# Optimization experiments

Hardware: AMD Instinct MI355X
Metric: run time of the kernel (lower is better)

Reference implementation:

```python
import jax, jax.numpy as jnp
import numpy as np

VOCAB = 50000
E = 32            # embed_size; node state is E x E
LABELS = 10
DEPTH = 11        # perfect binary tree: 2^DEPTH - 1 = 2047 nodes, 1024 leaves
N_NODES = 2 ** DEPTH - 1
LN_EPS = 1e-5


def setup_inputs() -> dict:
    key = jax.random.key(0)
    ks = jax.random.split(key, 8)
    word_ids = jax.random.randint(ks[0], (N_NODES,), 0, VOCAB, dtype=jnp.int32)
    label = 3
    emb_table = jax.random.normal(ks[1], (VOCAB, E * E), dtype=jnp.float32) * 0.02
    Ww = jax.random.normal(ks[2], (E, E), dtype=jnp.float32) * (1.0 / np.sqrt(E))
    Wb = jax.random.normal(ks[3], (E,), dtype=jnp.float32) * 0.01
    gamma = jnp.ones((E, E), dtype=jnp.float32)   # LayerNorm((1,E,E)) affine weight
    beta = jnp.zeros((E, E), dtype=jnp.float32)
    Pw = jax.random.normal(ks[4], (LABELS, E * E), dtype=jnp.float32) * (1.0 / E)
    Pb = jnp.zeros((LABELS,), dtype=jnp.float32)
    return {"word_ids": word_ids, "label": label, "emb_table": emb_table,
            "Ww": Ww, "Wb": Wb, "gamma": gamma, "beta": beta, "Pw": Pw, "Pb": Pb}


def reference(word_ids, label, emb_table, Ww, Wb, gamma, beta, Pw, Pb):
    # word_ids: level-order ids of a perfect binary tree, children of within-level
    # index j at level d are indices 2j, 2j+1 at level d+1.
    embs = emb_table[word_ids].reshape(N_NODES, E, E)  # [N, E, E]

    def ln_relu(x):
        # torch LayerNorm((1,E,E)): normalize over the whole E*E matrix, affine per element
        mu = jnp.mean(x, axis=(1, 2), keepdims=True)
        var = jnp.var(x, axis=(1, 2), keepdims=True)
        y = (x - mu) * jax.lax.rsqrt(var + LN_EPS) * gamma + beta
        return jax.nn.relu(y)

    # leaves: level DEPTH-1
    start = 2 ** (DEPTH - 1) - 1
    h = ln_relu(embs[start:])  # [2^(DEPTH-1), E, E]
    # internal levels bottom-up; loop over fixed DEPTH-1 levels (not data dims)
    for d in range(DEPTH - 2, -1, -1):
        s = 2 ** d - 1
        cur = embs[s:s + 2 ** d]                     # [n_d, E, E]
        l, r = h[0::2], h[1::2]                      # children pairs
        x = jnp.einsum('nij,njk,nkl->nil', l, r, cur)
        x = x @ Ww.T + Wb                            # Linear applied row-wise
        h = ln_relu(x)

    root = h[0].reshape(-1)                          # [E*E]
    logits = root @ Pw.T + Pb                        # [LABELS]
    prediction = jnp.argmax(logits)
    loss = -jax.nn.log_softmax(logits)[label]
    return (prediction, loss)
```

## Files before the change

kernel.cpp:

```cpp
#include <hip/hip_runtime.h>
#include <hip/hip_bf16.h>

#define LN_EPS 1e-5f
#define TSB 40
#define TILEB (32 * TSB)
#define MAGIC 0x5A5A7E1Du

typedef __attribute__((ext_vector_type(8))) short bf16x8;
typedef __attribute__((ext_vector_type(16))) float f32x16;

__device__ __forceinline__ short bf16b(float f) {
  return __builtin_bit_cast(short, __float2bfloat16(f));
}

__device__ __forceinline__ void wave_reduce2(float& s1, float& s2) {
  #pragma unroll
  for (int off = 32; off; off >>= 1) {
    s1 += __shfl_xor(s1, off);
    s2 += __shfl_xor(s2, off);
  }
}

__device__ __forceinline__ bf16x8 frag_ld(const short* t, int l, int k0) {
  return *(const bf16x8*)&t[(l & 31) * TSB + ((l >> 5) << 3) + k0];
}

__device__ __forceinline__ int cd_row(int r, int l) {
  return (r & 3) + 8 * (r >> 2) + 4 * (l >> 5);
}

__device__ __forceinline__ void cd_store(short* t, int l, const f32x16 d,
                                         bool transp) {
  const int col = l & 31;
  if (transp) {
    #pragma unroll
    for (int r = 0; r < 16; ++r) t[col * TSB + cd_row(r, l)] = bf16b(d[r]);
  } else {
    #pragma unroll
    for (int r = 0; r < 16; ++r) t[cd_row(r, l) * TSB + col] = bf16b(d[r]);
  }
}

struct NodeParams {
  bf16x8 w0, w1;
  float wb;
  float ga[16], be[16];
};

__device__ __forceinline__ NodeParams load_params(const float* __restrict__ Ww,
    const float* __restrict__ Wb, const float* __restrict__ gamma,
    const float* __restrict__ beta, int l) {
  NodeParams P;
  const int n = l & 31, kh = (l >> 5) * 8;
  float w[8];
  *(float4*)&w[0] = *(const float4*)&Ww[n * 32 + kh];
  *(float4*)&w[4] = *(const float4*)&Ww[n * 32 + kh + 4];
  #pragma unroll
  for (int i = 0; i < 8; ++i) P.w0[i] = bf16b(w[i]);
  *(float4*)&w[0] = *(const float4*)&Ww[n * 32 + kh + 16];
  *(float4*)&w[4] = *(const float4*)&Ww[n * 32 + kh + 20];
  #pragma unroll
  for (int i = 0; i < 8; ++i) P.w1[i] = bf16b(w[i]);
  P.wb = Wb[n];
  #pragma unroll
  for (int r = 0; r < 16; ++r) {
    const int idx = cd_row(r, l) * 32 + n;
    P.ga[r] = gamma[idx];
    P.be[r] = beta[idx];
  }
  return P;
}

__device__ __forceinline__ f32x16 mm32(const short* A, const short* B, int l) {
  f32x16 acc = {};
  acc = __builtin_amdgcn_mfma_f32_32x32x16_bf16(frag_ld(A, l, 0),
                                                frag_ld(B, l, 0), acc, 0, 0, 0);
  acc = __builtin_amdgcn_mfma_f32_32x32x16_bf16(frag_ld(A, l, 16),
                                                frag_ld(B, l, 16), acc, 0, 0, 0);
  return acc;
}

__device__ __forceinline__ void node_mfma(short* A, short* Bt, const short* Ct,
                                          const NodeParams& P, int l,
                                          short* dst, bool transpOut,
                                          float* fout) {
  f32x16 t1 = mm32(A, Bt, l);
  cd_store(A, l, t1, false);
  f32x16 t2 = mm32(A, Ct, l);
  cd_store(Bt, l, t2, false);
  f32x16 x = {};
  x = __builtin_amdgcn_mfma_f32_32x32x16_bf16(frag_ld(Bt, l, 0), P.w0, x, 0, 0, 0);
  x = __builtin_amdgcn_mfma_f32_32x32x16_bf16(frag_ld(Bt, l, 16), P.w1, x, 0, 0, 0);
  float s1 = 0.f, s2 = 0.f;
  #pragma unroll
  for (int r = 0; r < 16; ++r) {
    x[r] += P.wb;
    s1 += x[r];
    s2 += x[r] * x[r];
  }
  wave_reduce2(s1, s2);
  const float mu = s1 * (1.f / 1024.f);
  const float rs = rsqrtf(s2 * (1.f / 1024.f) - mu * mu + LN_EPS);
  #pragma unroll
  for (int r = 0; r < 16; ++r)
    x[r] = fmaxf((x[r] - mu) * rs * P.ga[r] + P.be[r], 0.f);
  if (fout) {
    #pragma unroll
    for (int r = 0; r < 16; ++r) fout[cd_row(r, l) * 32 + (l & 31)] = x[r];
  } else {
    cd_store(dst, l, x, transpOut);
  }
}

__device__ __forceinline__ void stage_f32(short* dst,
                                          const float* __restrict__ src, int l,
                                          bool transp) {
  float v[16];
  #pragma unroll
  for (int q = 0; q < 4; ++q)
    *(float4*)&v[q * 4] = *(const float4*)&src[l * 16 + q * 4];
  const int row = l >> 1, c0 = (l & 1) * 16;
  if (transp) {
    #pragma unroll
    for (int i = 0; i < 16; ++i) dst[(c0 + i) * TSB + row] = bf16b(v[i]);
  } else {
    #pragma unroll
    for (int i = 0; i < 8; ++i) {
      unsigned lo = (unsigned short)bf16b(v[2 * i]);
      unsigned hi = (unsigned short)bf16b(v[2 * i + 1]);
      ((unsigned*)dst)[row * (TSB / 2) + (c0 >> 1) + i] = lo | (hi << 16);
    }
  }
}

__device__ __forceinline__ void lds_put16(short* dst, const short v[16], int l,
                                          bool transp) {
  const int row = l >> 1, c0 = (l & 1) * 16;
  if (transp) {
    #pragma unroll
    for (int i = 0; i < 16; ++i) dst[(c0 + i) * TSB + row] = v[i];
  } else {
    #pragma unroll
    for (int i = 0; i < 8; ++i) {
      unsigned lo = (unsigned short)v[2 * i];
      unsigned hi = (unsigned short)v[2 * i + 1];
      ((unsigned*)dst)[row * (TSB / 2) + (c0 >> 1) + i] = lo | (hi << 16);
    }
  }
}

__device__ __forceinline__ void fetch_tile(short* dstLds,
                                           const unsigned* __restrict__ src,
                                           int l, bool transp) {
  short v[16];
  #pragma unroll
  for (int i = 0; i < 8; ++i) {
    unsigned x = __hip_atomic_load(src + l * 8 + i, __ATOMIC_RELAXED,
                                   __HIP_MEMORY_SCOPE_AGENT);
    v[2 * i] = (short)(x & 0xFFFFu);
    v[2 * i + 1] = (short)(x >> 16);
  }
  lds_put16(dstLds, v, l, transp);
}

__device__ __forceinline__ void emit_tile(unsigned* __restrict__ dst,
                                          const short* t, int u) {
  #pragma unroll
  for (int q = 0; q < 2; ++q) {
    const int w = 2 * u + q;
    const int row = w >> 4, cp = w & 15;
    unsigned v = *(const unsigned*)&t[row * TSB + cp * 2];
    __hip_atomic_store(dst + w, v, __ATOMIC_RELAXED, __HIP_MEMORY_SCOPE_AGENT);
  }
}

__device__ __forceinline__ void flag_set(unsigned* f) {
  __hip_atomic_store(f, MAGIC, __ATOMIC_RELAXED, __HIP_MEMORY_SCOPE_AGENT);
}

__device__ __forceinline__ void flag_wait(const unsigned* f) {
  while (__hip_atomic_load(f, __ATOMIC_RELAXED, __HIP_MEMORY_SCOPE_AGENT) !=
         MAGIC)
    __builtin_amdgcn_s_sleep(1);
  asm volatile("" ::: "memory");
}

__device__ __forceinline__ void leaf_ln(short* dst, const float* __restrict__ src,
                                        const float* __restrict__ gamma,
                                        const float* __restrict__ beta, int l,
                                        bool transp) {
  float v[16], ga[16], be[16];
  #pragma unroll
  for (int q = 0; q < 4; ++q) {
    *(float4*)&v[q * 4] = *(const float4*)&src[l * 16 + q * 4];
    *(float4*)&ga[q * 4] = *(const float4*)&gamma[l * 16 + q * 4];
    *(float4*)&be[q * 4] = *(const float4*)&beta[l * 16 + q * 4];
  }
  float s1 = 0.f, s2 = 0.f;
  #pragma unroll
  for (int i = 0; i < 16; ++i) { s1 += v[i]; s2 += v[i] * v[i]; }
  wave_reduce2(s1, s2);
  const float mu = s1 * (1.f / 1024.f);
  const float rs = rsqrtf(s2 * (1.f / 1024.f) - mu * mu + LN_EPS);
  short o[16];
  #pragma unroll
  for (int i = 0; i < 16; ++i)
    o[i] = bf16b(fmaxf((v[i] - mu) * rs * ga[i] + be[i], 0.f));
  lds_put16(dst, o, l, transp);
}

__device__ __forceinline__ void phase3(
    int blk, int u, int wv, int l, short* pool, const NodeParams& P,
    const int* __restrict__ wid, const float* __restrict__ emb,
    const unsigned* __restrict__ hinu, const unsigned* __restrict__ finf,
    unsigned* __restrict__ houtu, unsigned* __restrict__ foutf,
    int b0, int b1, int b2) {
  stage_f32(pool + (8 + wv) * TILEB,
            emb + (size_t)wid[b0 + 4 * blk + wv] * 1024, l, true);
  if (wv < 2)
    stage_f32(pool + (12 + wv) * TILEB,
              emb + (size_t)wid[b1 + 2 * blk + wv] * 1024, l, true);
  else if (wv == 2)
    stage_f32(pool + 14 * TILEB, emb + (size_t)wid[b2 + blk] * 1024, l, true);
  if (u < 8) flag_wait(finf + 8 * blk + u);
  __syncthreads();
  fetch_tile(pool + 2 * wv * TILEB, hinu + (size_t)(8 * blk + 2 * wv) * 512, l,
             false);
  fetch_tile(pool + (2 * wv + 1) * TILEB,
             hinu + (size_t)(8 * blk + 2 * wv + 1) * 512, l, true);
  __syncthreads();
  node_mfma(pool + 2 * wv * TILEB, pool + (2 * wv + 1) * TILEB,
            pool + (8 + wv) * TILEB, P, l, pool + (8 + wv) * TILEB,
            (wv & 1) != 0, nullptr);
  __syncthreads();
  if (wv < 2)
    node_mfma(pool + (8 + 2 * wv) * TILEB, pool + (9 + 2 * wv) * TILEB,
              pool + (12 + wv) * TILEB, P, l, pool + (12 + wv) * TILEB,
              (wv & 1) != 0, nullptr);
  __syncthreads();
  if (wv == 0)
    node_mfma(pool + 12 * TILEB, pool + 13 * TILEB, pool + 14 * TILEB, P, l,
              pool + 14 * TILEB, false, nullptr);
  __syncthreads();
  emit_tile(houtu + (size_t)blk * 512, pool + 14 * TILEB, u);
  asm volatile("s_waitcnt vmcnt(0)" ::: "memory");
  __syncthreads();
  if (u == 0) flag_set(foutf + blk);
}

__global__ __launch_bounds__(256) void k_tree(
    const int* __restrict__ wid, const float* __restrict__ emb,
    const float* __restrict__ Ww, const float* __restrict__ Wb,
    const float* __restrict__ gamma, const float* __restrict__ beta,
    const float* __restrict__ Pw, const float* __restrict__ Pb,
    const int* __restrict__ label,
    unsigned* __restrict__ h8u, unsigned* __restrict__ h5u,
    unsigned* __restrict__ h2u, unsigned* __restrict__ h8f,
    unsigned* __restrict__ h5f, unsigned* __restrict__ h2f,
    float* __restrict__ out) {
  __shared__ __align__(16) short pool[15 * TILEB];
  __shared__ float rootf[1024];
  __shared__ float lred[10];
  const int u = threadIdx.x, blk = blockIdx.x;
  const int wv = u >> 6, l = u & 63;
  NodeParams P = load_params(Ww, Wb, gamma, beta, l);

  {
    if (wv == 0)
      stage_f32(pool + 4 * TILEB, emb + (size_t)wid[511 + 2 * blk] * 1024, l, true);
    else if (wv == 1)
      stage_f32(pool + 5 * TILEB, emb + (size_t)wid[512 + 2 * blk] * 1024, l, true);
    else if (wv == 2)
      stage_f32(pool + 6 * TILEB, emb + (size_t)wid[255 + blk] * 1024, l, true);
    leaf_ln(pool + wv * TILEB, emb + (size_t)wid[1023 + 4 * blk + wv] * 1024,
            gamma, beta, l, (wv & 1) != 0);
    __syncthreads();
    if (wv < 2)
      node_mfma(pool + 2 * wv * TILEB, pool + (2 * wv + 1) * TILEB,
                pool + (4 + wv) * TILEB, P, l, pool + (4 + wv) * TILEB,
                wv == 1, nullptr);
    __syncthreads();
    if (wv == 0)
      node_mfma(pool + 4 * TILEB, pool + 5 * TILEB, pool + 6 * TILEB, P, l,
                pool + 6 * TILEB, false, nullptr);
    __syncthreads();
    emit_tile(h8u + (size_t)blk * 512, pool + 6 * TILEB, u);
    asm volatile("s_waitcnt vmcnt(0)" ::: "memory");
    __syncthreads();
    if (u == 0) flag_set(h8f + blk);
  }

  if (blk >= 32) return;
  phase3(blk, u, wv, l, pool, P, wid, emb, h8u, h8f, h5u, h5f, 127, 63, 31);

  if (blk >= 4) return;
  phase3(blk, u, wv, l, pool, P, wid, emb, h5u, h5f, h2u, h2f, 15, 7, 3);

  if (blk >= 1) return;
  {
    if (wv == 0) stage_f32(pool + 4 * TILEB, emb + (size_t)wid[1] * 1024, l, true);
    else if (wv == 1) stage_f32(pool + 5 * TILEB, emb + (size_t)wid[2] * 1024, l, true);
    else if (wv == 2) stage_f32(pool + 6 * TILEB, emb + (size_t)wid[0] * 1024, l, true);
    if (u < 4) flag_wait(h2f + u);
    __syncthreads();
    fetch_tile(pool + wv * TILEB, h2u + (size_t)wv * 512, l, (wv & 1) != 0);
    __syncthreads();
    if (wv < 2)
      node_mfma(pool + 2 * wv * TILEB, pool + (2 * wv + 1) * TILEB,
                pool + (4 + wv) * TILEB, P, l, pool + (4 + wv) * TILEB, wv == 1,
                nullptr);
    __syncthreads();
    if (wv == 0)
      node_mfma(pool + 4 * TILEB, pool + 5 * TILEB, pool + 6 * TILEB, P, l,
                nullptr, false, rootf);
    __syncthreads();
    #pragma unroll
    for (int q = 0; q < 3; ++q) {
      const int c = wv + 4 * q;
      if (c < 10) {
        float p = 0.f;
        #pragma unroll
        for (int t = 0; t < 4; ++t) {
          float4 r4 = *(const float4*)&rootf[l * 16 + t * 4];
          float4 w4 = *(const float4*)&Pw[c * 1024 + l * 16 + t * 4];
          p += r4.x * w4.x + r4.y * w4.y + r4.z * w4.z + r4.w * w4.w;
        }
        #pragma unroll
        for (int off = 32; off; off >>= 1) p += __shfl_xor(p, off);
        if (l == 0) lred[c] = p + Pb[c];
      }
    }
    __syncthreads();
    if (u == 0) {
      float mmax = lred[0];
      int am = 0;
      #pragma unroll
      for (int c = 1; c < 10; ++c)
        if (lred[c] > mmax) { mmax = lred[c]; am = c; }
      float sum = 0.f;
      #pragma unroll
      for (int c = 0; c < 10; ++c) sum += expf(lred[c] - mmax);
      const float loss = -(lred[label[0]] - mmax - logf(sum));
      out[0] = (float)am;
      out[1] = loss;
    }
  }
}

extern "C" void kernel_launch(void* const* d_in, const int* in_sizes, int n_in,
                              void* d_out, int out_size, void* d_ws, size_t ws_size,
                              hipStream_t stream) {
  const int* wid = (const int*)d_in[0];
  const int* label = (const int*)d_in[1];
  const float* emb = (const float*)d_in[2];
  const float* Ww = (const float*)d_in[3];
  const float* Wb = (const float*)d_in[4];
  const float* g = (const float*)d_in[5];
  const float* b = (const float*)d_in[6];
  const float* Pw = (const float*)d_in[7];
  const float* Pb = (const float*)d_in[8];
  float* out = (float*)d_out;

  unsigned* h8u = (unsigned*)d_ws;
  unsigned* h5u = h8u + 256 * 512;
  unsigned* h2u = h5u + 32 * 512;
  unsigned* h8f = h2u + 4 * 512;
  unsigned* h5f = h8f + 256;
  unsigned* h2f = h5f + 32;

  k_tree<<<256, 256, 0, stream>>>(wid, emb, Ww, Wb, g, b, Pw, Pb, label,
                                  h8u, h5u, h2u, h8f, h5f, h2f, out);
}
```

Before: 31.73 us.

## Precompute cur·Wᵀ per node and collapse tree into two-phase 32-block kernel

```diff
diff --git a/kernel.cpp b/kernel.cpp
--- a/kernel.cpp
+++ b/kernel.cpp
@@ -80,38 +80,6 @@
   return acc;
 }
 
-__device__ __forceinline__ void node_mfma(short* A, short* Bt, const short* Ct,
-                                          const NodeParams& P, int l,
-                                          short* dst, bool transpOut,
-                                          float* fout) {
-  f32x16 t1 = mm32(A, Bt, l);
-  cd_store(A, l, t1, false);
-  f32x16 t2 = mm32(A, Ct, l);
-  cd_store(Bt, l, t2, false);
-  f32x16 x = {};
-  x = __builtin_amdgcn_mfma_f32_32x32x16_bf16(frag_ld(Bt, l, 0), P.w0, x, 0, 0, 0);
-  x = __builtin_amdgcn_mfma_f32_32x32x16_bf16(frag_ld(Bt, l, 16), P.w1, x, 0, 0, 0);
-  float s1 = 0.f, s2 = 0.f;
-  #pragma unroll
-  for (int r = 0; r < 16; ++r) {
-    x[r] += P.wb;
-    s1 += x[r];
-    s2 += x[r] * x[r];
-  }
-  wave_reduce2(s1, s2);
-  const float mu = s1 * (1.f / 1024.f);
-  const float rs = rsqrtf(s2 * (1.f / 1024.f) - mu * mu + LN_EPS);
-  #pragma unroll
-  for (int r = 0; r < 16; ++r)
-    x[r] = fmaxf((x[r] - mu) * rs * P.ga[r] + P.be[r], 0.f);
-  if (fout) {
-    #pragma unroll
-    for (int r = 0; r < 16; ++r) fout[cd_row(r, l) * 32 + (l & 31)] = x[r];
-  } else {
-    cd_store(dst, l, x, transpOut);
-  }
-}
-
 __device__ __forceinline__ void stage_f32(short* dst,
                                           const float* __restrict__ src, int l,
                                           bool transp) {
@@ -133,6 +101,43 @@
   }
 }
 
+__device__ __forceinline__ void cw_prep(short* slot,
+                                        const float* __restrict__ src,
+                                        const NodeParams& P, int l) {
+  stage_f32(slot, src, l, false);
+  f32x16 cw = {};
+  cw = __builtin_amdgcn_mfma_f32_32x32x16_bf16(frag_ld(slot, l, 0), P.w0, cw, 0, 0, 0);
+  cw = __builtin_amdgcn_mfma_f32_32x32x16_bf16(frag_ld(slot, l, 16), P.w1, cw, 0, 0, 0);
+  cd_store(slot, l, cw, true);
+}
+
+__device__ __forceinline__ void node2(short* A, short* Bt, short* CWt,
+                                      const NodeParams& P, int l, short* dst,
+                                      bool transpOut, float* fout) {
+  f32x16 t1 = mm32(A, Bt, l);
+  cd_store(A, l, t1, false);
+  f32x16 x = mm32(A, CWt, l);
+  float s1 = 0.f, s2 = 0.f;
+  #pragma unroll
+  for (int r = 0; r < 16; ++r) {
+    x[r] += P.wb;
+    s1 += x[r];
+    s2 += x[r] * x[r];
+  }
+  wave_reduce2(s1, s2);
+  const float mu = s1 * (1.f / 1024.f);
+  const float rs = rsqrtf(s2 * (1.f / 1024.f) - mu * mu + LN_EPS);
+  #pragma unroll
+  for (int r = 0; r < 16; ++r)
+    x[r] = fmaxf((x[r] - mu) * rs * P.ga[r] + P.be[r], 0.f);
+  if (fout) {
+    #pragma unroll
+    for (int r = 0; r < 16; ++r) fout[cd_row(r, l) * 32 + (l & 31)] = x[r];
+  } else {
+    cd_store(dst, l, x, transpOut);
+  }
+}
+
 __device__ __forceinline__ void lds_put16(short* dst, const short v[16], int l,
                                           bool transp) {
   const int row = l >> 1, c0 = (l & 1) * 16;
@@ -163,15 +168,11 @@
   lds_put16(dstLds, v, l, transp);
 }
 
-__device__ __forceinline__ void emit_tile(unsigned* __restrict__ dst,
-                                          const short* t, int u) {
-  #pragma unroll
-  for (int q = 0; q < 2; ++q) {
-    const int w = 2 * u + q;
-    const int row = w >> 4, cp = w & 15;
-    unsigned v = *(const unsigned*)&t[row * TSB + cp * 2];
-    __hip_atomic_store(dst + w, v, __ATOMIC_RELAXED, __HIP_MEMORY_SCOPE_AGENT);
-  }
+__device__ __forceinline__ void emit512(unsigned* __restrict__ dst,
+                                        const short* t, int u) {
+  const int row = u >> 4, cp = u & 15;
+  unsigned v = *(const unsigned*)&t[row * TSB + cp * 2];
+  __hip_atomic_store(dst + u, v, __ATOMIC_RELAXED, __HIP_MEMORY_SCOPE_AGENT);
 }
 
 __device__ __forceinline__ void flag_set(unsigned* f) {
@@ -209,141 +210,143 @@
   lds_put16(dst, o, l, transp);
 }
 
-__device__ __forceinline__ void phase3(
-    int blk, int u, int wv, int l, short* pool, const NodeParams& P,
-    const int* __restrict__ wid, const float* __restrict__ emb,
-    const unsigned* __restrict__ hinu, const unsigned* __restrict__ finf,
-    unsigned* __restrict__ houtu, unsigned* __restrict__ foutf,
-    int b0, int b1, int b2) {
-  stage_f32(pool + (8 + wv) * TILEB,
-            emb + (size_t)wid[b0 + 4 * blk + wv] * 1024, l, true);
-  if (wv < 2)
-    stage_f32(pool + (12 + wv) * TILEB,
-              emb + (size_t)wid[b1 + 2 * blk + wv] * 1024, l, true);
-  else if (wv == 2)
-    stage_f32(pool + 14 * TILEB, emb + (size_t)wid[b2 + blk] * 1024, l, true);
-  if (u < 8) flag_wait(finf + 8 * blk + u);
-  __syncthreads();
-  fetch_tile(pool + 2 * wv * TILEB, hinu + (size_t)(8 * blk + 2 * wv) * 512, l,
-             false);
-  fetch_tile(pool + (2 * wv + 1) * TILEB,
-             hinu + (size_t)(8 * blk + 2 * wv + 1) * 512, l, true);
-  __syncthreads();
-  node_mfma(pool + 2 * wv * TILEB, pool + (2 * wv + 1) * TILEB,
-            pool + (8 + wv) * TILEB, P, l, pool + (8 + wv) * TILEB,
-            (wv & 1) != 0, nullptr);
-  __syncthreads();
-  if (wv < 2)
-    node_mfma(pool + (8 + 2 * wv) * TILEB, pool + (9 + 2 * wv) * TILEB,
-              pool + (12 + wv) * TILEB, P, l, pool + (12 + wv) * TILEB,
-              (wv & 1) != 0, nullptr);
-  __syncthreads();
-  if (wv == 0)
-    node_mfma(pool + 12 * TILEB, pool + 13 * TILEB, pool + 14 * TILEB, P, l,
-              pool + 14 * TILEB, false, nullptr);
-  __syncthreads();
-  emit_tile(houtu + (size_t)blk * 512, pool + 14 * TILEB, u);
-  asm volatile("s_waitcnt vmcnt(0)" ::: "memory");
-  __syncthreads();
-  if (u == 0) flag_set(foutf + blk);
-}
-
-__global__ __launch_bounds__(256) void k_tree(
+__global__ __launch_bounds__(512) void k_tree2(
     const int* __restrict__ wid, const float* __restrict__ emb,
     const float* __restrict__ Ww, const float* __restrict__ Wb,
     const float* __restrict__ gamma, const float* __restrict__ beta,
     const float* __restrict__ Pw, const float* __restrict__ Pb,
-    const int* __restrict__ label,
-    unsigned* __restrict__ h8u, unsigned* __restrict__ h5u,
-    unsigned* __restrict__ h2u, unsigned* __restrict__ h8f,
-    unsigned* __restrict__ h5f, unsigned* __restrict__ h2f,
-    float* __restrict__ out) {
-  __shared__ __align__(16) short pool[15 * TILEB];
-  __shared__ float rootf[1024];
-  __shared__ float lred[10];
+    const int* __restrict__ label, unsigned* __restrict__ h5u,
+    unsigned* __restrict__ h5f, float* __restrict__ out) {
+  extern __shared__ __align__(16) short pool[];
   const int u = threadIdx.x, blk = blockIdx.x;
   const int wv = u >> 6, l = u & 63;
   NodeParams P = load_params(Ww, Wb, gamma, beta, l);
 
+  cw_prep(pool + (2 * wv) * TILEB,
+          emb + (size_t)wid[511 + 16 * blk + 2 * wv] * 1024, P, l);
+  cw_prep(pool + (2 * wv + 1) * TILEB,
+          emb + (size_t)wid[512 + 16 * blk + 2 * wv] * 1024, P, l);
+  cw_prep(pool + (16 + wv) * TILEB,
+          emb + (size_t)wid[255 + 8 * blk + wv] * 1024, P, l);
+  if (wv < 4)
+    cw_prep(pool + (24 + wv) * TILEB,
+            emb + (size_t)wid[127 + 4 * blk + wv] * 1024, P, l);
+  else if (wv < 6)
+    cw_prep(pool + (28 + (wv - 4)) * TILEB,
+            emb + (size_t)wid[63 + 2 * blk + (wv - 4)] * 1024, P, l);
+  else if (wv == 6)
+    cw_prep(pool + 30 * TILEB, emb + (size_t)wid[31 + blk] * 1024, P, l);
+
   {
-    if (wv == 0)
-      stage_f32(pool + 4 * TILEB, emb + (size_t)wid[511 + 2 * blk] * 1024, l, true);
-    else if (wv == 1)
-      stage_f32(pool + 5 * TILEB, emb + (size_t)wid[512 + 2 * blk] * 1024, l, true);
-    else if (wv == 2)
-      stage_f32(pool + 6 * TILEB, emb + (size_t)wid[255 + blk] * 1024, l, true);
-    leaf_ln(pool + wv * TILEB, emb + (size_t)wid[1023 + 4 * blk + wv] * 1024,
-            gamma, beta, l, (wv & 1) != 0);
-    __syncthreads();
-    if (wv < 2)
-      node_mfma(pool + 2 * wv * TILEB, pool + (2 * wv + 1) * TILEB,
-                pool + (4 + wv) * TILEB, P, l, pool + (4 + wv) * TILEB,
-                wv == 1, nullptr);
-    __syncthreads();
-    if (wv == 0)
-      node_mfma(pool + 4 * TILEB, pool + 5 * TILEB, pool + 6 * TILEB, P, l,
-                pool + 6 * TILEB, false, nullptr);
-    __syncthreads();
-    emit_tile(h8u + (size_t)blk * 512, pool + 6 * TILEB, u);
-    asm volatile("s_waitcnt vmcnt(0)" ::: "memory");
-    __syncthreads();
-    if (u == 0) flag_set(h8f + blk);
-  }
-
-  if (blk >= 32) return;
-  phase3(blk, u, wv, l, pool, P, wid, emb, h8u, h8f, h5u, h5f, 127, 63, 31);
-
-  if (blk >= 4) return;
-  phase3(blk, u, wv, l, pool, P, wid, emb, h5u, h5f, h2u, h2f, 15, 7, 3);
-
-  if (blk >= 1) return;
-  {
-    if (wv == 0) stage_f32(pool + 4 * TILEB, emb + (size_t)wid[1] * 1024, l, true);
-    else if (wv == 1) stage_f32(pool + 5 * TILEB, emb + (size_t)wid[2] * 1024, l, true);
-    else if (wv == 2) stage_f32(pool + 6 * TILEB, emb + (size_t)wid[0] * 1024, l, true);
-    if (u < 4) flag_wait(h2f + u);
-    __syncthreads();
-    fetch_tile(pool + wv * TILEB, h2u + (size_t)wv * 512, l, (wv & 1) != 0);
-    __syncthreads();
-    if (wv < 2)
-      node_mfma(pool + 2 * wv * TILEB, pool + (2 * wv + 1) * TILEB,
-                pool + (4 + wv) * TILEB, P, l, pool + (4 + wv) * TILEB, wv == 1,
-                nullptr);
-    __syncthreads();
-    if (wv == 0)
-      node_mfma(pool + 4 * TILEB, pool + 5 * TILEB, pool + 6 * TILEB, P, l,
-                nullptr, false, rootf);
-    __syncthreads();
-    #pragma unroll
-    for (int q = 0; q < 3; ++q) {
-      const int c = wv + 4 * q;
-      if (c < 10) {
-        float p = 0.f;
-        #pragma unroll
-        for (int t = 0; t < 4; ++t) {
-          float4 r4 = *(const float4*)&rootf[l * 16 + t * 4];
-          float4 w4 = *(const float4*)&Pw[c * 1024 + l * 16 + t * 4];
-          p += r4.x * w4.x + r4.y * w4.y + r4.z * w4.z + r4.w * w4.w;
-        }
-        #pragma unroll
-        for (int off = 32; off; off >>= 1) p += __shfl_xor(p, off);
-        if (l == 0) lred[c] = p + Pb[c];
+    short* Lf0 = pool + (31 + 2 * wv) * TILEB;
+    short* Lf1 = pool + (32 + 2 * wv) * TILEB;
+    const int lb = 1023 + 32 * blk + 4 * wv;
+    leaf_ln(Lf0, emb + (size_t)wid[lb] * 1024, gamma, beta, l, false);
+    leaf_ln(Lf1, emb + (size_t)wid[lb + 1] * 1024, gamma, beta, l, true);
+    node2(Lf0, Lf1, pool + (2 * wv) * TILEB, P, l, pool + (2 * wv) * TILEB,
+          false, nullptr);
+    leaf_ln(Lf0, emb + (size_t)wid[lb + 2] * 1024, gamma, beta, l, false);
+    leaf_ln(Lf1, emb + (size_t)wid[lb + 3] * 1024, gamma, beta, l, true);
+    node2(Lf0, Lf1, pool + (2 * wv + 1) * TILEB, P, l,
+          pool + (2 * wv + 1) * TILEB, true, nullptr);
+    node2(pool + (2 * wv) * TILEB, pool + (2 * wv + 1) * TILEB,
+          pool + (16 + wv) * TILEB, P, l, pool + (16 + wv) * TILEB,
+          (wv & 1) != 0, nullptr);
+  }
+  __syncthreads();
+  if (wv < 4)
+    node2(pool + (16 + 2 * wv) * TILEB, pool + (17 + 2 * wv) * TILEB,
+          pool + (24 + wv) * TILEB, P, l, pool + (24 + wv) * TILEB,
+          (wv & 1) != 0, nullptr);
+  __syncthreads();
+  if (wv < 2)
+    node2(pool + (24 + 2 * wv) * TILEB, pool + (25 + 2 * wv) * TILEB,
+          pool + (28 + wv) * TILEB, P, l, pool + (28 + wv) * TILEB,
+          (wv & 1) != 0, nullptr);
+  __syncthreads();
+  if (wv == 0)
+    node2(pool + 28 * TILEB, pool + 29 * TILEB, pool + 30 * TILEB, P, l,
+          pool + 30 * TILEB, false, nullptr);
+  __syncthreads();
+  emit512(h5u + (size_t)blk * 512, pool + 30 * TILEB, u);
+  asm volatile("s_waitcnt vmcnt(0)" ::: "memory");
+  __syncthreads();
+  if (u == 0) flag_set(h5f + blk);
+
+  if (blk != 0) return;
+  cw_prep(pool + (32 + 2 * wv) * TILEB, emb + (size_t)wid[15 + 2 * wv] * 1024,
+          P, l);
+  cw_prep(pool + (33 + 2 * wv) * TILEB, emb + (size_t)wid[16 + 2 * wv] * 1024,
+          P, l);
+  cw_prep(pool + (48 + wv) * TILEB, emb + (size_t)wid[7 + wv] * 1024, P, l);
+  if (wv < 4)
+    cw_prep(pool + (56 + wv) * TILEB, emb + (size_t)wid[3 + wv] * 1024, P, l);
+  else if (wv < 6)
+    cw_prep(pool + (60 + (wv - 4)) * TILEB,
+            emb + (size_t)wid[1 + (wv - 4)] * 1024, P, l);
+  else if (wv == 6)
+    cw_prep(pool + 62 * TILEB, emb + (size_t)wid[0] * 1024, P, l);
+  if (u < 32) flag_wait(h5f + u);
+  __syncthreads();
+  #pragma unroll
+  for (int q = 0; q < 4; ++q)
+    fetch_tile(pool + (4 * wv + q) * TILEB, h5u + (size_t)(4 * wv + q) * 512,
+               l, (q & 1) != 0);
+  node2(pool + (4 * wv) * TILEB, pool + (4 * wv + 1) * TILEB,
+        pool + (32 + 2 * wv) * TILEB, P, l, pool + (32 + 2 * wv) * TILEB,
+        false, nullptr);
+  node2(pool + (4 * wv + 2) * TILEB, pool + (4 * wv + 3) * TILEB,
+        pool + (33 + 2 * wv) * TILEB, P, l, pool + (33 + 2 * wv) * TILEB,
+        true, nullptr);
+  node2(pool + (32 + 2 * wv) * TILEB, pool + (33 + 2 * wv) * TILEB,
+        pool + (48 + wv) * TILEB, P, l, pool + (48 + wv) * TILEB,
+        (wv & 1) != 0, nullptr);
+  __syncthreads();
+  if (wv < 4)
+    node2(pool + (48 + 2 * wv) * TILEB, pool + (49 + 2 * wv) * TILEB,
+          pool + (56 + wv) * TILEB, P, l, pool + (56 + wv) * TILEB,
+          (wv & 1) != 0, nullptr);
+  __syncthreads();
+  if (wv < 2)
+    node2(pool + (56 + 2 * wv) * TILEB, pool + (57 + 2 * wv) * TILEB,
+          pool + (60 + wv) * TILEB, P, l, pool + (60 + wv) * TILEB,
+          (wv & 1) != 0, nullptr);
+  __syncthreads();
+  float* rootf = (float*)pool;
+  float* lred = (float*)pool + 1024;
+  if (wv == 0)
+    node2(pool + 60 * TILEB, pool + 61 * TILEB, pool + 62 * TILEB, P, l,
+          nullptr, false, rootf);
+  __syncthreads();
+  #pragma unroll
+  for (int q = 0; q < 2; ++q) {
+    const int c = wv + 8 * q;
+    if (c < 10) {
+      float p = 0.f;
+      #pragma unroll
+      for (int t = 0; t < 4; ++t) {
+        float4 r4 = *(const float4*)&rootf[l * 16 + t * 4];
+        float4 w4 = *(const float4*)&Pw[c * 1024 + l * 16 + t * 4];
+        p += r4.x * w4.x + r4.y * w4.y + r4.z * w4.z + r4.w * w4.w;
       }
+      #pragma unroll
+      for (int off = 32; off; off >>= 1) p += __shfl_xor(p, off);
+      if (l == 0) lred[c] = p + Pb[c];
     }
-    __syncthreads();
-    if (u == 0) {
-      float mmax = lred[0];
-      int am = 0;
-      #pragma unroll
-      for (int c = 1; c < 10; ++c)
-        if (lred[c] > mmax) { mmax = lred[c]; am = c; }
-      float sum = 0.f;
-      #pragma unroll
-      for (int c = 0; c < 10; ++c) sum += expf(lred[c] - mmax);
-      const float loss = -(lred[label[0]] - mmax - logf(sum));
-      out[0] = (float)am;
-      out[1] = loss;
-    }
+  }
+  __syncthreads();
+  if (u == 0) {
+    float mmax = lred[0];
+    int am = 0;
+    #pragma unroll
+    for (int c = 1; c < 10; ++c)
+      if (lred[c] > mmax) { mmax = lred[c]; am = c; }
+    float sum = 0.f;
+    #pragma unroll
+    for (int c = 0; c < 10; ++c) sum += expf(lred[c] - mmax);
+    const float loss = -(lred[label[0]] - mmax - logf(sum));
+    out[0] = (float)am;
+    out[1] = loss;
   }
 }
 
@@ -361,13 +364,13 @@
   const float* Pb = (const float*)d_in[8];
   float* out = (float*)d_out;
 
-  unsigned* h8u = (unsigned*)d_ws;
-  unsigned* h5u = h8u + 256 * 512;
-  unsigned* h2u = h5u + 32 * 512;
-  unsigned* h8f = h2u + 4 * 512;
-  unsigned* h5f = h8f + 256;
-  unsigned* h2f = h5f + 32;
-
-  k_tree<<<256, 256, 0, stream>>>(wid, emb, Ww, Wb, g, b, Pw, Pb, label,
-                                  h8u, h5u, h2u, h8f, h5f, h2f, out);
-}
+  unsigned* h5u = (unsigned*)d_ws;
+  unsigned* h5f = h5u + 32 * 512;
+
+  const size_t SMEM = 63 * TILEB * sizeof(short);
+  (void)hipFuncSetAttribute((const void*)k_tree2,
+                            hipFuncAttributeMaxDynamicSharedMemorySize,
+                            (int)SMEM);
+  k_tree2<<<32, 512, SMEM, stream>>>(wid, emb, Ww, Wb, g, b, Pw, Pb, label,
+                                     h5u, h5f, out);
+}
```

After: 35.71 us. 1.13x slower.
